# Performance work log

Hardware: AMD Instinct MI355X
Metric: run time of the kernel (lower is better)

## Reference

```python
import jax, jax.numpy as jnp
import numpy as np

N = 6144      # number of pedestrians
HID = 256     # hidden_dim
OUT = 32      # out_dim
NTOP = 4      # n nearest neighbours
EMB = OUT // NTOP  # per-neighbour embedding dim = 8


def setup_inputs() -> dict:
    key = jax.random.key(0)
    ks = jax.random.split(key, 12)
    r = lambda k, shp, s=1.0: (jax.random.normal(k, shp, dtype=jnp.float32) * s)
    return {
        "obs1": r(ks[0], (N, 2)),
        "obs2": r(ks[1], (N, 2)),
        "h": r(ks[2], (N, HID), 0.1),
        "c": r(ks[3], (N, HID), 0.1),
        "W_emb": r(ks[4], (4, EMB), 0.3),
        "b_emb": r(ks[5], (EMB,), 0.1),
        "W_ih": r(ks[6], (4 * HID, OUT), 0.1),
        "b_ih": r(ks[7], (4 * HID,), 0.1),
        "W_hh": r(ks[8], (4 * HID, HID), 0.1),
        "b_hh": r(ks[9], (4 * HID,), 0.1),
        "W_pool": r(ks[10], (OUT, HID), 0.1),
        "b_pool": r(ks[11], (OUT,), 0.1),
    }


def reference(obs1, obs2, h, c, W_emb, b_emb, W_ih, b_ih, W_hh, b_hh, W_pool, b_pool):
    n = obs2.shape[0]
    vel = obs2 - obs1                                   # [N,2]
    # rel_position[i, j] = obs2[j] - obs2[i]
    diff = obs2[None, :, :] - obs2[:, None, :]          # [N,N,2]
    dist = jnp.linalg.norm(diff, axis=-1)               # [N,N]
    # exclude self (torch code drops the diagonal before topk)
    dist = jnp.where(jnp.eye(n, dtype=bool), jnp.inf, dist)
    _, idx = jax.lax.top_k(-dist, NTOP)                 # [N,NTOP] indices of nearest
    nearest_pos = jnp.take_along_axis(diff, idx[:, :, None], axis=1)  # [N,NTOP,2]
    # rel_direction[i, j] = vel[j] - vel[i]
    nearest_vel = vel[idx] - vel[:, None, :]            # [N,NTOP,2]
    feat = jnp.concatenate([nearest_pos, nearest_vel], axis=-1)       # [N,NTOP,4]
    # Linear(4, EMB) + ReLU, then flatten neighbours -> [N, OUT]
    emb = jax.nn.relu(feat @ W_emb + b_emb).reshape(n, -1)
    # LSTMCell (PyTorch gate order: i, f, g, o)
    gates = emb @ W_ih.T + b_ih + h @ W_hh.T + b_hh     # [N,4*HID]
    gi, gf, gg, go = jnp.split(gates, 4, axis=-1)
    c_new = jax.nn.sigmoid(gf) * c + jax.nn.sigmoid(gi) * jnp.tanh(gg)
    h_new = jax.nn.sigmoid(go) * jnp.tanh(c_new)
    out = h_new @ W_pool.T + b_pool                     # [N,OUT]
    return out
```

## Files before the change

### kernel.cpp

```cpp
#include <hip/hip_runtime.h>
#include <math.h>

typedef unsigned short u16;
typedef unsigned long long u64;
typedef __attribute__((ext_vector_type(8))) short bf16x8;
typedef __attribute__((ext_vector_type(4))) float f32x4;

__device__ __forceinline__ float sigf(float x)  { return 1.0f / (1.0f + __expf(-x)); }
__device__ __forceinline__ float tanhf_(float x){ float e = __expf(2.0f * x); return 1.0f - 2.0f / (e + 1.0f); }
__device__ __forceinline__ u16 f2bf(float f) {
    unsigned x = __float_as_uint(f);
    return (u16)((x + 0x7fffu + ((x >> 16) & 1u)) >> 16);
}

#define INSU(KEY) do {                                                              \
    u64 _k = (KEY);                                                                 \
    k3 = (_k < k3) ? _k : k3;                                                       \
    { bool _c = k3 < k2; u64 _lo = _c ? k3 : k2, _hi = _c ? k2 : k3; k2 = _lo; k3 = _hi; } \
    { bool _c = k2 < k1; u64 _lo = _c ? k2 : k1, _hi = _c ? k1 : k2; k1 = _lo; k2 = _hi; } \
    { bool _c = k1 < k0; u64 _lo = _c ? k1 : k0, _hi = _c ? k0 : k1; k0 = _lo; k1 = _hi; } \
} while (0)

#define INS4(D, J) do {                                                              \
    float _d = (D); int _j = (J);                                                    \
    if (_d < bd3 || (_d == bd3 && _j < bj3)) {                                       \
        bd3 = _d; bj3 = _j;                                                          \
        if (bd3 < bd2 || (bd3 == bd2 && bj3 < bj2)) {                                \
            float _t = bd2; bd2 = bd3; bd3 = _t; int _u = bj2; bj2 = bj3; bj3 = _u; }\
        if (bd2 < bd1 || (bd2 == bd1 && bj2 < bj1)) {                                \
            float _t = bd1; bd1 = bd2; bd2 = _t; int _u = bj1; bj1 = bj2; bj2 = _u; }\
        if (bd1 < bd0 || (bd1 == bd0 && bj1 < bj0)) {                                \
            float _t = bd0; bd0 = bd1; bd1 = _t; int _u = bj0; bj0 = bj1; bj1 = _u; }\
    } } while (0)

__global__ void diag_kernel(float* out, int code, int out_size) {
    if (out_size > 0) out[0] = (float)code * 1.0e8f;
}

__global__ __launch_bounds__(256) void knn_prep_kernel(
    const float* __restrict__ obs1, const float* __restrict__ obs2,
    const float* __restrict__ Wemb, const float* __restrict__ bemb,
    const float* __restrict__ Wih,  const float* __restrict__ Whh,
    const float* __restrict__ Wp,
    u16* __restrict__ Wgf, u16* __restrict__ Wpf,
    int n, int knn_blocks, float* __restrict__ out)
{
    const int t = threadIdx.x;

    if (blockIdx.x >= knn_blocks) {
        int id = (blockIdx.x - knn_blocks) * 256 + t;
        if (id < 36864) {
            int gt = id / 576, rem = id - gt * 576;
            int kt = rem >> 6, ln = rem & 63;
            int g  = gt * 16 + (ln & 15);
            int k  = kt * 32 + (ln >> 4) * 8;
            u16* dst = Wgf + (size_t)id * 8;
            #pragma unroll
            for (int j = 0; j < 8; j++) {
                int kk = k + j;
                float v = (kk < 32) ? Wih[(size_t)g * 32 + kk]
                                    : Whh[(size_t)g * 256 + (kk - 32)];
                dst[j] = f2bf(v);
            }
        } else if (id < 37888) {
            int id2 = id - 36864;
            int pt = id2 >> 9, rem = id2 & 511;
            int kt = rem >> 6, ln = rem & 63;
            int o  = pt * 16 + (ln & 15);
            int k  = kt * 32 + (ln >> 4) * 8;
            u16* dst = Wpf + (size_t)id2 * 8;
            #pragma unroll
            for (int j = 0; j < 8; j++)
                dst[j] = f2bf(Wp[(size_t)o * 256 + k + j]);
        }
        return;
    }

    const int lane = t & 63;
    const int wv   = t >> 6;
    const int i    = blockIdx.x * 4 + wv;
    if (i >= n) return;

    const float2* o2 = (const float2*)obs2;
    const float2 pi = o2[i];

    u64 k0 = ~0ull, k1 = ~0ull, k2 = ~0ull, k3 = ~0ull;

    int j = lane;
    for (; j + 192 < n; j += 256) {
        float2 p0 = o2[j], p1 = o2[j + 64], p2 = o2[j + 128], p3 = o2[j + 192];
        float dx, dy, d2; u64 key;
        dx = p0.x - pi.x; dy = p0.y - pi.y;
        d2 = __fadd_rn(__fmul_rn(dx, dx), __fmul_rn(dy, dy));
        key = (((u64)__float_as_uint(d2)) << 24) | (unsigned)j;
        key = (j == i) ? ~0ull : key;                         INSU(key);
        dx = p1.x - pi.x; dy = p1.y - pi.y;
        d2 = __fadd_rn(__fmul_rn(dx, dx), __fmul_rn(dy, dy));
        key = (((u64)__float_as_uint(d2)) << 24) | (unsigned)(j + 64);
        key = (j + 64 == i) ? ~0ull : key;                    INSU(key);
        dx = p2.x - pi.x; dy = p2.y - pi.y;
        d2 = __fadd_rn(__fmul_rn(dx, dx), __fmul_rn(dy, dy));
        key = (((u64)__float_as_uint(d2)) << 24) | (unsigned)(j + 128);
        key = (j + 128 == i) ? ~0ull : key;                   INSU(key);
        dx = p3.x - pi.x; dy = p3.y - pi.y;
        d2 = __fadd_rn(__fmul_rn(dx, dx), __fmul_rn(dy, dy));
        key = (((u64)__float_as_uint(d2)) << 24) | (unsigned)(j + 192);
        key = (j + 192 == i) ? ~0ull : key;                   INSU(key);
    }
    for (; j < n; j += 64) {
        float2 pj = o2[j];
        float dx = pj.x - pi.x, dy = pj.y - pi.y;
        float d2 = __fadd_rn(__fmul_rn(dx, dx), __fmul_rn(dy, dy));
        u64 key = (((u64)__float_as_uint(d2)) << 24) | (unsigned)j;
        key = (j == i) ? ~0ull : key;
        INSU(key);
    }

    #pragma unroll
    for (int m = 1; m < 64; m <<= 1) {
        u64 o0 = __shfl_xor(k0, m), o1 = __shfl_xor(k1, m);
        u64 o2_ = __shfl_xor(k2, m), o3 = __shfl_xor(k3, m);
        INSU(o0); INSU(o1); INSU(o2_); INSU(o3);
    }

    if (lane < 4) {
        u64 kq = (lane == 0) ? k0 : (lane == 1) ? k1 : (lane == 2) ? k2 : k3;
        int jn = (int)(kq & 0xFFFFFF);
        if (jn < 0 || jn >= n) jn = 0;
        float pix = pi.x, piy = pi.y;
        float pjx = obs2[2 * jn], pjy = obs2[2 * jn + 1];
        float px = pjx - pix, py = pjy - piy;
        float vix = pix - obs1[2 * i];
        float viy = piy - obs1[2 * i + 1];
        float vx = (pjx - obs1[2 * jn])     - vix;
        float vy = (pjy - obs1[2 * jn + 1]) - viy;
        float* dst = out + (size_t)i * 32 + lane * 8;
        #pragma unroll
        for (int e = 0; e < 8; e++) {
            float a = px * Wemb[e]      + py * Wemb[8 + e]
                    + vx * Wemb[16 + e] + vy * Wemb[24 + e]
                    + bemb[e];
            dst[e] = fmaxf(a, 0.0f);
        }
    }
}

__global__ __launch_bounds__(1024) void lstm_kernel(
    const float* __restrict__ h,   const float* __restrict__ c,
    const u16*  __restrict__ Wgf,  const float* __restrict__ bih,
    const float* __restrict__ bhh,
    const u16*  __restrict__ Wpf,  const float* __restrict__ bp,
    int n, float* __restrict__ out)
{
    __shared__ __align__(16) char lds[17920];
    u16* sXb = (u16*)lds;
    u16* sHb = (u16*)(lds + 9472);

    const int t    = threadIdx.x;
    const int i0   = blockIdx.x * 16;
    const int lane = t & 63;
    const int wv   = t >> 6;
    const int fm   = lane & 15;
    const int fq   = lane >> 4;

    if (t < 512) {
        int r = t >> 5, e = t & 31;
        int row = i0 + r;
        float v = (row < n) ? out[(size_t)row * 32 + e] : 0.0f;
        sXb[r * 296 + e] = f2bf(v);
    }
    {
        int r = t >> 6, k4 = t & 63;
        int row = i0 + r;
        float4 hv = (row < n) ? ((const float4*)h)[(size_t)row * 64 + k4]
                              : make_float4(0.f, 0.f, 0.f, 0.f);
        u16* d = &sXb[r * 296 + 32 + k4 * 4];
        d[0] = f2bf(hv.x); d[1] = f2bf(hv.y); d[2] = f2bf(hv.z); d[3] = f2bf(hv.w);
    }
    __syncthreads();

    bf16x8 afr[9];
    #pragma unroll
    for (int kt = 0; kt < 9; kt++)
        afr[kt] = *(const bf16x8*)&sXb[fm * 296 + kt * 32 + fq * 8];

    {
        const int ut = wv;
        const int u  = ut * 16 + fm;

        f32x4 acc[4];
        #pragma unroll
        for (int jg = 0; jg < 4; jg++) acc[jg] = (f32x4){0.f, 0.f, 0.f, 0.f};

        #pragma unroll
        for (int jg = 0; jg < 4; jg++) {
            const int gt = jg * 16 + ut;
            const u16* wbase = Wgf + ((size_t)gt * 9) * 512 + lane * 8;
            #pragma unroll
            for (int kt = 0; kt < 9; kt++) {
                bf16x8 bfr = *(const bf16x8*)(wbase + kt * 512);
                acc[jg] = __builtin_amdgcn_mfma_f32_16x16x32_bf16(afr[kt], bfr, acc[jg], 0, 0, 0);
            }
        }

        float b0 = bih[u]       + bhh[u];
        float b1 = bih[u + 256] + bhh[u + 256];
        float b2 = bih[u + 512] + bhh[u + 512];
        float b3 = bih[u + 768] + bhh[u + 768];

        #pragma unroll
        for (int r_ = 0; r_ < 4; r_++) {
            int row = i0 + fq * 4 + r_;
            float cin = (row < n) ? c[(size_t)row * 256 + u] : 0.0f;
            float gi = acc[0][r_] + b0;
            float gf = acc[1][r_] + b1;
            float gg = acc[2][r_] + b2;
            float go = acc[3][r_] + b3;
            float cn = sigf(gf) * cin + sigf(gi) * tanhf_(gg);
            float hn = sigf(go) * tanhf_(cn);
            sHb[(fq * 4 + r_) * 264 + u] = f2bf(hn);
        }
    }
    __syncthreads();

    if (wv < 2) {
        bf16x8 ah[8];
        #pragma unroll
        for (int kt = 0; kt < 8; kt++)
            ah[kt] = *(const bf16x8*)&sHb[fm * 264 + kt * 32 + fq * 8];
        const u16* wbase = Wpf + ((size_t)wv * 8) * 512 + lane * 8;
        f32x4 acc = {0.f, 0.f, 0.f, 0.f};
        #pragma unroll
        for (int kt = 0; kt < 8; kt++) {
            bf16x8 bfr = *(const bf16x8*)(wbase + kt * 512);
            acc = __builtin_amdgcn_mfma_f32_16x16x32_bf16(ah[kt], bfr, acc, 0, 0, 0);
        }
        float bias = bp[wv * 16 + fm];
        #pragma unroll
        for (int r_ = 0; r_ < 4; r_++) {
            int row = i0 + fq * 4 + r_;
            if (row < n) out[(size_t)row * 32 + wv * 16 + fm] = acc[r_] + bias;
        }
    }
}

__global__ __launch_bounds__(256) void nnlstm_fallback(
    const float* __restrict__ obs1, const float* __restrict__ obs2,
    const float* __restrict__ h,    const float* __restrict__ c,
    const float* __restrict__ Wemb, const float* __restrict__ bemb,
    const float* __restrict__ Wih,  const float* __restrict__ bih,
    const float* __restrict__ Whh,  const float* __restrict__ bhh,
    const float* __restrict__ Wp,   const float* __restrict__ bp,
    int n, float* __restrict__ out)
{
    __shared__ float sMd[16][64];
    __shared__ int   sMj[16][64];
    __shared__ float sX[16][292];
    __shared__ float sH[16][264];

    const int t   = threadIdx.x;
    const int sub = t & 15;
    const int ii  = t >> 4;
    const int i0  = blockIdx.x * 16;
    const int i   = i0 + ii;

    for (int v = t; v < 16 * 256; v += 256) {
        int r = v >> 8, k = v & 255;
        int row = i0 + r;
        sX[r][32 + k] = (row < n) ? h[(size_t)row * 256 + k] : 0.0f;
    }

    float bd0 = 1e30f, bd1 = 1e30f, bd2 = 1e30f, bd3 = 1e30f;
    int   bj0 = 0x7fffffff, bj1 = 0x7fffffff, bj2 = 0x7fffffff, bj3 = 0x7fffffff;

    if (i < n) {
        const float pix = obs2[2 * i];
        const float piy = obs2[2 * i + 1];
        for (int j = sub; j < n; j += 16) {
            float dx = obs2[2 * j]     - pix;
            float dy = obs2[2 * j + 1] - piy;
            float d2 = __fadd_rn(__fmul_rn(dx, dx), __fmul_rn(dy, dy));
            float dist = __fsqrt_rn(d2);
            if (j == i) continue;
            INS4(dist, j);
        }
    }
    sMd[ii][sub * 4 + 0] = bd0;  sMj[ii][sub * 4 + 0] = bj0;
    sMd[ii][sub * 4 + 1] = bd1;  sMj[ii][sub * 4 + 1] = bj1;
    sMd[ii][sub * 4 + 2] = bd2;  sMj[ii][sub * 4 + 2] = bj2;
    sMd[ii][sub * 4 + 3] = bd3;  sMj[ii][sub * 4 + 3] = bj3;
    __syncthreads();

    if (t < 16) {
        const int r = t;
        const int irow = i0 + r;
        float bd0 = 1e30f, bd1 = 1e30f, bd2 = 1e30f, bd3 = 1e30f;
        int   bj0 = 0x7fffffff, bj1 = 0x7fffffff, bj2 = 0x7fffffff, bj3 = 0x7fffffff;
        for (int q = 0; q < 64; q++) { INS4(sMd[r][q], sMj[r][q]); }

        if (irow < n) {
            float pix = obs2[2 * irow], piy = obs2[2 * irow + 1];
            float vix = pix - obs1[2 * irow];
            float viy = piy - obs1[2 * irow + 1];
            #pragma unroll
            for (int q2 = 0; q2 < 4; q2++) {
                int jn = (q2 == 0) ? bj0 : (q2 == 1) ? bj1 : (q2 == 2) ? bj2 : bj3;
                if (jn < 0 || jn >= n) jn = 0;
                float pjx = obs2[2 * jn], pjy = obs2[2 * jn + 1];
                float px = pjx - pix, py = pjy - piy;
                float vx = (pjx - obs1[2 * jn])     - vix;
                float vy = (pjy - obs1[2 * jn + 1]) - viy;
                #pragma unroll
                for (int e = 0; e < 8; e++) {
                    float a = px * Wemb[e]      + py * Wemb[8 + e]
                            + vx * Wemb[16 + e] + vy * Wemb[24 + e]
                            + bemb[e];
                    sX[r][q2 * 8 + e] = fmaxf(a, 0.0f);
                }
            }
        } else {
            for (int e = 0; e < 32; e++) sX[r][e] = 0.0f;
        }
    }
    __syncthreads();

    const int uu = t;
    float acc[4][16];
    #pragma unroll
    for (int j = 0; j < 4; j++) {
        float b = bih[uu + 256 * j] + bhh[uu + 256 * j];
        #pragma unroll
        for (int r = 0; r < 16; r++) acc[j][r] = b;
    }

    for (int kc = 0; kc < 288; kc++) {
        float w[4];
        #pragma unroll
        for (int j = 0; j < 4; j++) {
            int g = uu + 256 * j;
            w[j] = (kc < 32) ? Wih[(size_t)g * 32 + kc]
                             : Whh[(size_t)g * 256 + (kc - 32)];
        }
        #pragma unroll
        for (int r = 0; r < 16; r++) {
            float x = sX[r][kc];
            #pragma unroll
            for (int j = 0; j < 4; j++) acc[j][r] += w[j] * x;
        }
    }

    for (int r = 0; r < 16; r++) {
        int row = i0 + r;
        float cin = (row < n) ? c[(size_t)row * 256 + uu] : 0.0f;
        float cn = sigf(acc[1][r]) * cin + sigf(acc[0][r]) * tanhf(acc[2][r]);
        float hn = sigf(acc[3][r]) * tanhf(cn);
        sH[r][uu] = hn;
    }
    __syncthreads();

    for (int v = t; v < 16 * 32; v += 256) {
        int r = v >> 5, o = v & 31;
        int row = i0 + r;
        if (row >= n) continue;
        float a = bp[o];
        for (int kc = 0; kc < 256; kc++)
            a += Wp[(size_t)o * 256 + kc] * sH[r][kc];
        out[(size_t)row * 32 + o] = a;
    }
}

extern "C" void kernel_launch(void* const* d_in, const int* in_sizes, int n_in,
                              void* d_out, int out_size, void* d_ws, size_t ws_size,
                              hipStream_t stream) {
    float* out = (float*)d_out;

    int code = 0, n = 0;
    if (n_in != 12) code = 1;
    else {
        n = in_sizes[1] / 2;
        if (n <= 4 || in_sizes[1] != 2 * n)          code = 2;
        else if (in_sizes[0]  != 2 * n)              code = 3;
        else if (in_sizes[2]  != 256 * n)            code = 4;
        else if (in_sizes[3]  != 256 * n)            code = 5;
        else if (in_sizes[4]  != 32 || in_sizes[5] != 8)        code = 6;
        else if (in_sizes[6]  != 32768 || in_sizes[7] != 1024)  code = 7;
        else if (in_sizes[8]  != 262144 || in_sizes[9] != 1024) code = 8;
        else if (in_sizes[10] != 8192 || in_sizes[11] != 32)    code = 9;
        else if (out_size != 32 * n)                 code = 10;
    }
    if (code != 0) {
        diag_kernel<<<1, 1, 0, stream>>>(out, code, out_size);
        return;
    }

    const float* obs1   = (const float*)d_in[0];
    const float* obs2   = (const float*)d_in[1];
    const float* h      = (const float*)d_in[2];
    const float* c      = (const float*)d_in[3];
    const float* W_emb  = (const float*)d_in[4];
    const float* b_emb  = (const float*)d_in[5];
    const float* W_ih   = (const float*)d_in[6];
    const float* b_ih   = (const float*)d_in[7];
    const float* W_hh   = (const float*)d_in[8];
    const float* b_hh   = (const float*)d_in[9];
    const float* W_pool = (const float*)d_in[10];
    const float* b_pool = (const float*)d_in[11];

    const size_t wgf_bytes = (size_t)36864 * 8 * sizeof(u16);
    const size_t wpf_bytes = (size_t)1024 * 8 * sizeof(u16);

    if (ws_size >= wgf_bytes + wpf_bytes && n <= (1 << 24)) {
        u16* Wgf = (u16*)d_ws;
        u16* Wpf = (u16*)((char*)d_ws + wgf_bytes);
        int knn_blocks = (n + 3) / 4;
        knn_prep_kernel<<<knn_blocks + 148, 256, 0, stream>>>(
            obs1, obs2, W_emb, b_emb, W_ih, W_hh, W_pool, Wgf, Wpf,
            n, knn_blocks, out);
        lstm_kernel<<<(n + 15) / 16, 1024, 0, stream>>>(
            h, c, Wgf, b_ih, b_hh, Wpf, b_pool, n, out);
    } else {
        nnlstm_fallback<<<(n + 15) / 16, 256, 0, stream>>>(
            obs1, obs2, h, c, W_emb, b_emb, W_ih, b_ih, W_hh, b_hh,
            W_pool, b_pool, n, out);
    }
}
```

Measured before the change: 147.8 us.

## Fuse kNN/weight-prep and LSTM kernels into one cooperative kernel with grid sync

Merges the kNN-plus-weight-packing kernel and the LSTM kernel into a single cooperative launch, separated by a grid-wide barrier, to remove the second launch and the gap between kernels. The LSTM phase now uses 256-thread blocks, so each wave computes four hidden-unit tiles instead of one, and the launch bounds allow six blocks per CU. Before launching, the host queries device properties and occupancy on every call to confirm the whole grid can be co-resident, and keeps the two-kernel path as a fallback. The costs are the grid sync, less parallelism in the LSTM phase, possible register pressure from the occupancy bound, and extra host-side queries per call.

```diff
diff --git a/kernel.cpp b/kernel.cpp
--- a/kernel.cpp
+++ b/kernel.cpp
@@ -1,5 +1,8 @@
 #include <hip/hip_runtime.h>
+#include <hip/hip_cooperative_groups.h>
 #include <math.h>
+
+namespace cg = cooperative_groups;
 
 typedef unsigned short u16;
 typedef unsigned long long u64;
@@ -37,6 +40,217 @@
     if (out_size > 0) out[0] = (float)code * 1.0e8f;
 }
 
+__device__ __forceinline__ void prep_item(
+    int id, const float* Wih, const float* Whh, const float* Wp,
+    u16* Wgf, u16* Wpf)
+{
+    if (id < 36864) {
+        int gt = id / 576, rem = id - gt * 576;
+        int kt = rem >> 6, ln = rem & 63;
+        int g  = gt * 16 + (ln & 15);
+        int k  = kt * 32 + (ln >> 4) * 8;
+        u16* dst = Wgf + (size_t)id * 8;
+        #pragma unroll
+        for (int j = 0; j < 8; j++) {
+            int kk = k + j;
+            float v = (kk < 32) ? Wih[(size_t)g * 32 + kk]
+                                : Whh[(size_t)g * 256 + (kk - 32)];
+            dst[j] = f2bf(v);
+        }
+    } else if (id < 37888) {
+        int id2 = id - 36864;
+        int pt = id2 >> 9, rem = id2 & 511;
+        int kt = rem >> 6, ln = rem & 63;
+        int o  = pt * 16 + (ln & 15);
+        int k  = kt * 32 + (ln >> 4) * 8;
+        u16* dst = Wpf + (size_t)id2 * 8;
+        #pragma unroll
+        for (int j = 0; j < 8; j++)
+            dst[j] = f2bf(Wp[(size_t)o * 256 + k + j]);
+    }
+}
+
+__global__ __launch_bounds__(256, 6) void coop_kernel(
+    const float* __restrict__ obs1, const float* __restrict__ obs2,
+    const float* __restrict__ h,    const float* __restrict__ c,
+    const float* __restrict__ Wemb, const float* __restrict__ bemb,
+    const float* __restrict__ Wih,  const float* __restrict__ Whh,
+    const float* __restrict__ Wp,
+    const float* __restrict__ bih,  const float* __restrict__ bhh,
+    const float* __restrict__ bp,
+    u16* __restrict__ Wgf, u16* __restrict__ Wpf,
+    int n, int knn_blocks, float* __restrict__ out)
+{
+    __shared__ __align__(16) char lds[17920];
+    u16* sXb = (u16*)lds;
+    u16* sHb = (u16*)(lds + 9472);
+
+    const int t    = threadIdx.x;
+    const int lane = t & 63;
+    const int wv   = t >> 6;
+    const int fm   = lane & 15;
+    const int fq   = lane >> 4;
+
+    if (blockIdx.x < 148) {
+        int id = blockIdx.x * 256 + t;
+        prep_item(id, Wih, Whh, Wp, Wgf, Wpf);
+    }
+
+    {
+        const int i = blockIdx.x * 4 + wv;
+        if (blockIdx.x < knn_blocks && i < n) {
+            const float2* o2 = (const float2*)obs2;
+            const float2 pi = o2[i];
+
+            u64 k0 = ~0ull, k1 = ~0ull, k2 = ~0ull, k3 = ~0ull;
+
+            int j = lane;
+            for (; j + 192 < n; j += 256) {
+                float2 p0 = o2[j], p1 = o2[j + 64], p2 = o2[j + 128], p3 = o2[j + 192];
+                float dx, dy, d2; u64 key;
+                dx = p0.x - pi.x; dy = p0.y - pi.y;
+                d2 = __fadd_rn(__fmul_rn(dx, dx), __fmul_rn(dy, dy));
+                key = (((u64)__float_as_uint(d2)) << 24) | (unsigned)j;
+                key = (j == i) ? ~0ull : key;                         INSU(key);
+                dx = p1.x - pi.x; dy = p1.y - pi.y;
+                d2 = __fadd_rn(__fmul_rn(dx, dx), __fmul_rn(dy, dy));
+                key = (((u64)__float_as_uint(d2)) << 24) | (unsigned)(j + 64);
+                key = (j + 64 == i) ? ~0ull : key;                    INSU(key);
+                dx = p2.x - pi.x; dy = p2.y - pi.y;
+                d2 = __fadd_rn(__fmul_rn(dx, dx), __fmul_rn(dy, dy));
+                key = (((u64)__float_as_uint(d2)) << 24) | (unsigned)(j + 128);
+                key = (j + 128 == i) ? ~0ull : key;                   INSU(key);
+                dx = p3.x - pi.x; dy = p3.y - pi.y;
+                d2 = __fadd_rn(__fmul_rn(dx, dx), __fmul_rn(dy, dy));
+                key = (((u64)__float_as_uint(d2)) << 24) | (unsigned)(j + 192);
+                key = (j + 192 == i) ? ~0ull : key;                   INSU(key);
+            }
+            for (; j < n; j += 64) {
+                float2 pj = o2[j];
+                float dx = pj.x - pi.x, dy = pj.y - pi.y;
+                float d2 = __fadd_rn(__fmul_rn(dx, dx), __fmul_rn(dy, dy));
+                u64 key = (((u64)__float_as_uint(d2)) << 24) | (unsigned)j;
+                key = (j == i) ? ~0ull : key;
+                INSU(key);
+            }
+
+            #pragma unroll
+            for (int m = 1; m < 64; m <<= 1) {
+                u64 o0 = __shfl_xor(k0, m), o1 = __shfl_xor(k1, m);
+                u64 o2_ = __shfl_xor(k2, m), o3 = __shfl_xor(k3, m);
+                INSU(o0); INSU(o1); INSU(o2_); INSU(o3);
+            }
+
+            if (lane < 4) {
+                u64 kq = (lane == 0) ? k0 : (lane == 1) ? k1 : (lane == 2) ? k2 : k3;
+                int jn = (int)(kq & 0xFFFFFF);
+                if (jn < 0 || jn >= n) jn = 0;
+                float pix = pi.x, piy = pi.y;
+                float pjx = obs2[2 * jn], pjy = obs2[2 * jn + 1];
+                float px = pjx - pix, py = pjy - piy;
+                float vix = pix - obs1[2 * i];
+                float viy = piy - obs1[2 * i + 1];
+                float vx = (pjx - obs1[2 * jn])     - vix;
+                float vy = (pjy - obs1[2 * jn + 1]) - viy;
+                float* dst = out + (size_t)i * 32 + lane * 8;
+                #pragma unroll
+                for (int e = 0; e < 8; e++) {
+                    float a = px * Wemb[e]      + py * Wemb[8 + e]
+                            + vx * Wemb[16 + e] + vy * Wemb[24 + e]
+                            + bemb[e];
+                    dst[e] = fmaxf(a, 0.0f);
+                }
+            }
+        }
+    }
+
+    cg::this_grid().sync();
+
+    if (blockIdx.x >= (n + 15) / 16) return;
+    const int i0 = blockIdx.x * 16;
+
+    for (int v = t; v < 512; v += 256) {
+        int r = v >> 5, e = v & 31;
+        int row = i0 + r;
+        float val = (row < n) ? out[(size_t)row * 32 + e] : 0.0f;
+        sXb[r * 296 + e] = f2bf(val);
+    }
+    for (int f = t; f < 1024; f += 256) {
+        int r = f >> 6, k4 = f & 63;
+        int row = i0 + r;
+        float4 hv = (row < n) ? ((const float4*)h)[(size_t)row * 64 + k4]
+                              : make_float4(0.f, 0.f, 0.f, 0.f);
+        u16* d = &sXb[r * 296 + 32 + k4 * 4];
+        d[0] = f2bf(hv.x); d[1] = f2bf(hv.y); d[2] = f2bf(hv.z); d[3] = f2bf(hv.w);
+    }
+    __syncthreads();
+
+    bf16x8 afr[9];
+    #pragma unroll
+    for (int kt = 0; kt < 9; kt++)
+        afr[kt] = *(const bf16x8*)&sXb[fm * 296 + kt * 32 + fq * 8];
+
+    #pragma unroll
+    for (int ut2 = 0; ut2 < 4; ut2++) {
+        const int ut = wv * 4 + ut2;
+        const int u  = ut * 16 + fm;
+
+        f32x4 acc[4];
+        #pragma unroll
+        for (int jg = 0; jg < 4; jg++) acc[jg] = (f32x4){0.f, 0.f, 0.f, 0.f};
+
+        #pragma unroll
+        for (int jg = 0; jg < 4; jg++) {
+            const int gt = jg * 16 + ut;
+            const u16* wbase = Wgf + ((size_t)gt * 9) * 512 + lane * 8;
+            #pragma unroll
+            for (int kt = 0; kt < 9; kt++) {
+                bf16x8 bfr = *(const bf16x8*)(wbase + kt * 512);
+                acc[jg] = __builtin_amdgcn_mfma_f32_16x16x32_bf16(afr[kt], bfr, acc[jg], 0, 0, 0);
+            }
+        }
+
+        float b0 = bih[u]       + bhh[u];
+        float b1 = bih[u + 256] + bhh[u + 256];
+        float b2 = bih[u + 512] + bhh[u + 512];
+        float b3 = bih[u + 768] + bhh[u + 768];
+
+        #pragma unroll
+        for (int r_ = 0; r_ < 4; r_++) {
+            int row = i0 + fq * 4 + r_;
+            float cin = (row < n) ? c[(size_t)row * 256 + u] : 0.0f;
+            float gi = acc[0][r_] + b0;
+            float gf = acc[1][r_] + b1;
+            float gg = acc[2][r_] + b2;
+            float go = acc[3][r_] + b3;
+            float cn = sigf(gf) * cin + sigf(gi) * tanhf_(gg);
+            float hn = sigf(go) * tanhf_(cn);
+            sHb[(fq * 4 + r_) * 264 + u] = f2bf(hn);
+        }
+    }
+    __syncthreads();
+
+    if (wv < 2) {
+        bf16x8 ah[8];
+        #pragma unroll
+        for (int kt = 0; kt < 8; kt++)
+            ah[kt] = *(const bf16x8*)&sHb[fm * 264 + kt * 32 + fq * 8];
+        const u16* wbase = Wpf + ((size_t)wv * 8) * 512 + lane * 8;
+        f32x4 acc = {0.f, 0.f, 0.f, 0.f};
+        #pragma unroll
+        for (int kt = 0; kt < 8; kt++) {
+            bf16x8 bfr = *(const bf16x8*)(wbase + kt * 512);
+            acc = __builtin_amdgcn_mfma_f32_16x16x32_bf16(ah[kt], bfr, acc, 0, 0, 0);
+        }
+        float bias = bp[wv * 16 + fm];
+        #pragma unroll
+        for (int r_ = 0; r_ < 4; r_++) {
+            int row = i0 + fq * 4 + r_;
+            if (row < n) out[(size_t)row * 32 + wv * 16 + fm] = acc[r_] + bias;
+        }
+    }
+}
+
 __global__ __launch_bounds__(256) void knn_prep_kernel(
     const float* __restrict__ obs1, const float* __restrict__ obs2,
     const float* __restrict__ Wemb, const float* __restrict__ bemb,
@@ -49,30 +263,7 @@
 
     if (blockIdx.x >= knn_blocks) {
         int id = (blockIdx.x - knn_blocks) * 256 + t;
-        if (id < 36864) {
-            int gt = id / 576, rem = id - gt * 576;
-            int kt = rem >> 6, ln = rem & 63;
-            int g  = gt * 16 + (ln & 15);
-            int k  = kt * 32 + (ln >> 4) * 8;
-            u16* dst = Wgf + (size_t)id * 8;
-            #pragma unroll
-            for (int j = 0; j < 8; j++) {
-                int kk = k + j;
-                float v = (kk < 32) ? Wih[(size_t)g * 32 + kk]
-                                    : Whh[(size_t)g * 256 + (kk - 32)];
-                dst[j] = f2bf(v);
-            }
-        } else if (id < 37888) {
-            int id2 = id - 36864;
-            int pt = id2 >> 9, rem = id2 & 511;
-            int kt = rem >> 6, ln = rem & 63;
-            int o  = pt * 16 + (ln & 15);
-            int k  = kt * 32 + (ln >> 4) * 8;
-            u16* dst = Wpf + (size_t)id2 * 8;
-            #pragma unroll
-            for (int j = 0; j < 8; j++)
-                dst[j] = f2bf(Wp[(size_t)o * 256 + k + j]);
-        }
+        prep_item(id, Wih, Whh, Wp, Wgf, Wpf);
         return;
     }
 
@@ -409,18 +600,46 @@
     const size_t wgf_bytes = (size_t)36864 * 8 * sizeof(u16);
     const size_t wpf_bytes = (size_t)1024 * 8 * sizeof(u16);
 
-    if (ws_size >= wgf_bytes + wpf_bytes && n <= (1 << 24)) {
-        u16* Wgf = (u16*)d_ws;
-        u16* Wpf = (u16*)((char*)d_ws + wgf_bytes);
-        int knn_blocks = (n + 3) / 4;
-        knn_prep_kernel<<<knn_blocks + 148, 256, 0, stream>>>(
-            obs1, obs2, W_emb, b_emb, W_ih, W_hh, W_pool, Wgf, Wpf,
-            n, knn_blocks, out);
-        lstm_kernel<<<(n + 15) / 16, 1024, 0, stream>>>(
-            h, c, Wgf, b_ih, b_hh, Wpf, b_pool, n, out);
-    } else {
+    if (!(ws_size >= wgf_bytes + wpf_bytes && n <= (1 << 24))) {
         nnlstm_fallback<<<(n + 15) / 16, 256, 0, stream>>>(
             obs1, obs2, h, c, W_emb, b_emb, W_ih, b_ih, W_hh, b_hh,
             W_pool, b_pool, n, out);
-    }
-}
+        return;
+    }
+
+    u16* Wgf = (u16*)d_ws;
+    u16* Wpf = (u16*)((char*)d_ws + wgf_bytes);
+    int knn_blocks = (n + 3) / 4;
+    int grid = (knn_blocks > 148) ? knn_blocks : 148;
+
+    bool coop_ok = false;
+    {
+        int occ = 0;
+        hipDeviceProp_t prop;
+        if (hipGetDeviceProperties(&prop, 0) == hipSuccess &&
+            hipOccupancyMaxActiveBlocksPerMultiprocessor(
+                &occ, (const void*)coop_kernel, 256, 0) == hipSuccess) {
+            coop_ok = ((long long)occ * prop.multiProcessorCount >= grid);
+        }
+    }
+
+    if (coop_ok) {
+        void* args[] = {
+            (void*)&obs1, (void*)&obs2, (void*)&h, (void*)&c,
+            (void*)&W_emb, (void*)&b_emb,
+            (void*)&W_ih, (void*)&W_hh, (void*)&W_pool,
+            (void*)&b_ih, (void*)&b_hh, (void*)&b_pool,
+            (void*)&Wgf, (void*)&Wpf,
+            (void*)&n, (void*)&knn_blocks, (void*)&out
+        };
+        hipError_t le = hipLaunchCooperativeKernel(
+            (void*)coop_kernel, dim3(grid), dim3(256), args, 0, stream);
+        if (le == hipSuccess) return;
+    }
+
+    knn_prep_kernel<<<knn_blocks + 148, 256, 0, stream>>>(
+        obs1, obs2, W_emb, b_emb, W_ih, W_hh, W_pool, Wgf, Wpf,
+        n, knn_blocks, out);
+    lstm_kernel<<<(n + 15) / 16, 1024, 0, stream>>>(
+        h, c, Wgf, b_ih, b_hh, Wpf, b_pool, n, out);
+}
```

Result: no change. 147.8 us (-0.0%).
